# Kernel optimization log

Measured on AMD Instinct MI355X. Metric: run time of the kernel, lower is better.

The kernel has to match this reference:

```python
import jax, jax.numpy as jnp
import numpy as np

EPS = 1e-12  # matches torch.nn.functional.normalize default eps


def _l2norm_ch(x):
    # normalize over channel axis (dim=1), x: [B, D, N]
    n = jnp.sqrt(jnp.sum(x * x, axis=1, keepdims=True))
    return x / jnp.maximum(n, EPS)


def setup_inputs() -> dict:
    key = jax.random.key(0)
    k0, k1, kq, kk, kv = jax.random.split(key, 5)
    B, D, H, W = 8, 128, 64, 64
    return {
        "vol0": jax.random.normal(k0, (B, D, H, W), dtype=jnp.float32),
        "vol1": jax.random.normal(k1, (B, D, H, W), dtype=jnp.float32),
        "Wq": jax.random.normal(kq, (D, D), dtype=jnp.float32) * 0.05,
        "Wk": jax.random.normal(kk, (D, D), dtype=jnp.float32) * 0.05,
        "Wv": jax.random.normal(kv, (D, D), dtype=jnp.float32) * 0.05,
    }


def reference(vol0, vol1, Wq, Wk, Wv):
    B, D, H, W = vol0.shape
    N = H * W
    x0 = vol0.reshape(B, D, N)
    x1 = vol1.reshape(B, D, N)

    # 1x1 convs (bias=False) == channel matmuls; residual connections enabled
    q = jnp.einsum('od,bdn->bon', Wq, x0) + x0
    k = jnp.einsum('od,bdn->bon', Wk, x1) + x1
    v0 = jnp.einsum('od,bdn->bon', Wv, x0) + x0
    v1 = jnp.einsum('od,bdn->bon', Wv, x1) + x1

    # normalise dot product: L2-normalize over channel dim
    q = _l2norm_ch(q)
    k = _l2norm_ch(k)

    # correlation volume + row softmax: cvolume[b, n, m]
    cvolume = jax.nn.softmax(jnp.einsum('bdn,bdm->bnm', q, k), axis=2)

    # warp v1 by attention: v1w[b, d, n] = sum_m v1[b, d, m] * cvolume[b, n, m]
    v1w = jnp.einsum('bdm,bnm->bdn', v1, cvolume)

    # position encoder (meshgrid with 'ij' indexing, as legacy torch.meshgrid)
    u = jnp.linspace(-1.0, 1.0, H)
    v = jnp.linspace(-1.0, 1.0, W)
    uu, vv = jnp.meshgrid(u, v, indexing='ij')
    grid = jnp.stack([uu, vv], axis=0).reshape(2, N)  # [2, N]
    pos = jnp.einsum('cm,bnm->bcn', grid, cvolume)  # [B, 2, N]

    # max-score channel: [B, 1, N]
    max_score = jnp.max(cvolume, axis=2)[:, None, :]

    agg = jnp.concatenate([v0, v1w, pos, max_score], axis=1)  # [B, 2D+3, N]
    return agg.reshape(B, 2 * D + 3, H, W)
```

## Files before the change

kernel.cpp:

```cpp
#include <hip/hip_runtime.h>
#include <hip/hip_bf16.h>

#define B_   8
#define D_   128
#define N_   4096
#define CH   259

typedef short bf8 __attribute__((ext_vector_type(8)));
typedef float f4  __attribute__((ext_vector_type(4)));

typedef unsigned int as1_u32 __attribute__((address_space(1)));
typedef unsigned int as3_u32 __attribute__((address_space(3)));

__device__ __forceinline__ void gll16(const void* g, void* l) {
    __builtin_amdgcn_global_load_lds((as1_u32*)(unsigned long long)g,
                                     (as3_u32*)(unsigned int)(unsigned long long)l,
                                     16, 0, 0);
}

__device__ __forceinline__ unsigned short f2bf(float x) {
    unsigned int u = __float_as_uint(x);
    return (unsigned short)((u + 0x7FFFu + ((u >> 16) & 1u)) >> 16);
}

__device__ __forceinline__ unsigned int cvtpk(float lo, float hi) {
    unsigned int r;
    asm("v_cvt_pk_bf16_f32 %0, %1, %2" : "=v"(r) : "v"(lo), "v"(hi));
    return r;
}

__global__ void wconv_kernel(const float* __restrict__ Wq,
                             const float* __restrict__ Wk,
                             const float* __restrict__ Wv,
                             unsigned short* __restrict__ Wb) {
    const float* src = (blockIdx.x == 0) ? Wq : (blockIdx.x == 1) ? Wk : Wv;
    unsigned short* dst = Wb + (size_t)blockIdx.x * D_ * D_;
    for (int i = threadIdx.x; i < D_ * D_; i += blockDim.x) dst[i] = f2bf(src[i]);
}

__global__ __launch_bounds__(256, 2) void proj_kernel(
    const float* __restrict__ vol0, const float* __restrict__ vol1,
    const unsigned short* __restrict__ Wb, float* __restrict__ out,
    unsigned short* __restrict__ Qp, unsigned short* __restrict__ Kh,
    unsigned short* __restrict__ V2)
{
    __shared__ __align__(16) float xs[2][D_ * 64];

    const int tid  = threadIdx.x;
    const int wave = tid >> 6, lane = tid & 63;
    const int l15  = lane & 15, lh = lane >> 4;

    const int bid = blockIdx.x;
    const int swz = (bid & 7) * 64 + (bid >> 3);
    const int b   = swz >> 6;
    const int n0  = (swz & 63) * 64;

    #pragma unroll
    for (int a = 0; a < 2; ++a) {
        const char* src = (const char*)((a ? vol1 : vol0) + (size_t)b * D_ * N_ + n0);
        char* dstb = (char*)&xs[a][0];
        #pragma unroll
        for (int i = 0; i < 8; ++i) {
            int dst16 = i * 4096 + tid * 16;
            int row = dst16 >> 8, cb = dst16 & 255;
            gll16(src + (size_t)row * (N_ * 4) + (cb ^ (((row >> 3) & 7) << 4)), dstb + dst16);
        }
    }
    __syncthreads();

    const int nrow = wave * 16 + l15;

    auto afrag = [&](const float* base, int k) -> bf8 {
        const int dbase = k * 32 + lh * 8;
        const unsigned int cb = ((unsigned int)(nrow * 4)) ^ (((unsigned int)((k * 4 + lh) & 7)) << 4);
        const float* p = base + dbase * 64 + (cb >> 2);
        union { bf8 v; unsigned int w[4]; } u;
        #pragma unroll
        for (int jj = 0; jj < 4; ++jj)
            u.w[jj] = cvtpk(p[(2 * jj) * 64], p[(2 * jj + 1) * 64]);
        return u.v;
    };

    f4 aq[8], ak[8], a0v[8], a1v[8];
    #pragma unroll
    for (int ob = 0; ob < 8; ++ob) {
        aq[ob] = (f4){0.f,0.f,0.f,0.f}; ak[ob] = (f4){0.f,0.f,0.f,0.f};
        a0v[ob] = (f4){0.f,0.f,0.f,0.f}; a1v[ob] = (f4){0.f,0.f,0.f,0.f};
    }

    const unsigned short* Wqb = Wb;
    const unsigned short* Wkb = Wb + D_ * D_;
    const unsigned short* Wvb = Wb + 2 * D_ * D_;

    for (int k = 0; k < 4; ++k) {
        bf8 x0f = afrag(&xs[0][0], k);
        bf8 x1f = afrag(&xs[1][0], k);
        #pragma unroll
        for (int ob = 0; ob < 8; ++ob) {
            const size_t woff = ((size_t)(ob * 16 + l15)) * D_ + k * 32 + lh * 8;
            bf8 wq = *(const bf8*)(Wqb + woff);
            bf8 wk = *(const bf8*)(Wkb + woff);
            bf8 wv = *(const bf8*)(Wvb + woff);
            aq[ob]  = __builtin_amdgcn_mfma_f32_16x16x32_bf16(x0f, wq, aq[ob], 0, 0, 0);
            ak[ob]  = __builtin_amdgcn_mfma_f32_16x16x32_bf16(x1f, wk, ak[ob], 0, 0, 0);
            a0v[ob] = __builtin_amdgcn_mfma_f32_16x16x32_bf16(x0f, wv, a0v[ob], 0, 0, 0);
            a1v[ob] = __builtin_amdgcn_mfma_f32_16x16x32_bf16(x1f, wv, a1v[ob], 0, 0, 0);
        }
    }

    float ssq[4] = {0.f,0.f,0.f,0.f}, ssk[4] = {0.f,0.f,0.f,0.f};
    #pragma unroll
    for (int ob = 0; ob < 8; ++ob) {
        const int o = ob * 16 + l15;
        const unsigned int okey = (((unsigned int)((o >> 3) & 7)) << 4);
        #pragma unroll
        for (int r = 0; r < 4; ++r) {
            int n = wave * 16 + lh * 4 + r;
            int ci = o * 64 + (int)(((((unsigned int)(n * 4)) ^ okey) >> 2));
            float r0 = xs[0][ci], r1 = xs[1][ci];
            aq[ob][r] += r0; ak[ob][r] += r1; a0v[ob][r] += r0; a1v[ob][r] += r1;
            ssq[r] = fmaf(aq[ob][r], aq[ob][r], ssq[r]);
            ssk[r] = fmaf(ak[ob][r], ak[ob][r], ssk[r]);
        }
    }
    #pragma unroll
    for (int off = 1; off < 16; off <<= 1)
        #pragma unroll
        for (int r = 0; r < 4; ++r) {
            ssq[r] += __shfl_xor(ssq[r], off, 64);
            ssk[r] += __shfl_xor(ssk[r], off, 64);
        }
    float rq[4], rk[4];
    #pragma unroll
    for (int r = 0; r < 4; ++r) {
        rq[r] = 1.44269504088896f / fmaxf(sqrtf(ssq[r]), 1e-12f);
        rk[r] = 1.0f / fmaxf(sqrtf(ssk[r]), 1e-12f);
    }

    const int nbase = n0 + wave * 16 + lh * 4;
    char* v2chunk = (char*)V2 + ((size_t)(b * 128 + (nbase >> 5))) * 8192
                  + (nbase & 31) * 2;

    #pragma unroll
    for (int ob = 0; ob < 8; ++ob) {
        const int o = ob * 16 + l15;
        *(f4*)(out + ((size_t)(b * CH + o)) * N_ + nbase) = a0v[ob];
        uint2 pv; pv.x = cvtpk(a1v[ob][0], a1v[ob][1]); pv.y = cvtpk(a1v[ob][2], a1v[ob][3]);
        *(uint2*)(v2chunk + (size_t)o * 64) = pv;
        uint2 pq; pq.x = cvtpk(aq[ob][0]*rq[0], aq[ob][1]*rq[1]);
        pq.y = cvtpk(aq[ob][2]*rq[2], aq[ob][3]*rq[3]);
        *(uint2*)(Qp + ((size_t)(b * D_ + o)) * N_ + nbase) = pq;
    }

    __syncthreads();
    float* chunk = &xs[0][0] + wave * 2176;
    #pragma unroll
    for (int ob = 0; ob < 8; ++ob) {
        const int o = ob * 16 + l15;
        #pragma unroll
        for (int r = 0; r < 4; ++r) chunk[o * 17 + lh * 4 + r] = ak[ob][r] * rk[r];
    }
    asm volatile("s_waitcnt lgkmcnt(0)" ::: "memory");
    __builtin_amdgcn_sched_barrier(0);
    {
        const int o0 = (lane & 15) * 8, nr = lane >> 4;
        #pragma unroll
        for (int t = 0; t < 4; ++t) {
            int nl = t * 4 + nr;
            float f[8];
            #pragma unroll
            for (int j = 0; j < 8; ++j) f[j] = chunk[(o0 + j) * 17 + nl];
            uint4 st;
            st.x = cvtpk(f[0], f[1]); st.y = cvtpk(f[2], f[3]);
            st.z = cvtpk(f[4], f[5]); st.w = cvtpk(f[6], f[7]);
            *(uint4*)(Kh + ((size_t)(b * N_ + n0 + wave * 16 + nl)) * D_ + o0) = st;
        }
    }
}

__global__ __launch_bounds__(512, 2) void attn_kernel(
    const unsigned short* __restrict__ Qp, const unsigned short* __restrict__ Kh,
    const unsigned short* __restrict__ V2, float* __restrict__ out)
{
    __shared__ __align__(16) char smem[81920];
    char* KB = smem;
    char* VB = smem + 32768;
    char* PB = smem + 65536;

    const int tid  = threadIdx.x;
    const int wave = tid >> 6, lane = tid & 63;
    const int l15  = lane & 15, lh = lane >> 4;
    const int mhalf = wave & 1, qquad = wave >> 1;

    const int bid = blockIdx.x;
    const int swz = (bid & 7) * 32 + (bid >> 3);
    const int b   = swz >> 5;
    const int n0  = (swz & 31) * 128;
    const int nw  = n0 + qquad * 32;

    bf8 qf[2][4];
    const unsigned short* Qb = Qp + (size_t)b * D_ * N_;
    #pragma unroll
    for (int qg = 0; qg < 2; ++qg)
        #pragma unroll
        for (int dc = 0; dc < 4; ++dc) {
            union { bf8 v; unsigned short e[8]; } u;
            #pragma unroll
            for (int j = 0; j < 8; ++j)
                u.e[j] = Qb[((size_t)(dc * 32 + lh * 8 + j)) * N_ + nw + qg * 16 + l15];
            qf[qg][dc] = u.v;
        }

    f4 acc[2][8];
    #pragma unroll
    for (int qg = 0; qg < 2; ++qg)
        #pragma unroll
        for (int dc = 0; dc < 8; ++dc) acc[qg][dc] = (f4){0.f,0.f,0.f,0.f};
    float lsum[2] = {0.f, 0.f}, pu[2] = {0.f, 0.f}, pvv[2] = {0.f, 0.f};
    float Mp[2] = {-1e30f, -1e30f};

    float vb0[8];
    #pragma unroll
    for (int s = 0; s < 2; ++s)
        #pragma unroll
        for (int r = 0; r < 4; ++r)
            vb0[s * 4 + r] = -1.f + (2.f / 63.f) * (float)(s * 16 + lh * 4 + r);

    const char* Kbytes = (const char*)(Kh + (size_t)b * N_ * D_);
    const char* Vbytes = (const char*)V2 + ((size_t)b * 128) * 8192;
    char* Pw = PB + wave * 2048;

    const int sK = (wave < 4);
    const int smh = sK ? (wave >> 1) : ((wave - 4) >> 1);
    const int spt = sK ? (wave & 1) : ((wave - 4) & 1);
    unsigned int soffs[4];
    #pragma unroll
    for (int ii = 0; ii < 4; ++ii) {
        if (sK) {
            int rr = spt * 16 + ii * 4 + (lane >> 4);
            unsigned int col = (unsigned int)((lane & 15) * 16);
            soffs[ii] = (unsigned int)(rr * 256) + (col ^ (unsigned int)((rr & 7) << 4));
        } else {
            int vr = spt * 64 + ii * 16 + (lane >> 2);
            unsigned int mc = (unsigned int)((lane & 3) * 16);
            soffs[ii] = (unsigned int)(vr * 64) + (mc ^ (unsigned int)(((vr >> 1) & 3) << 4));
        }
    }
    auto stage = [&](int buf, int t) {
        if (sK) {
            const char* ks = Kbytes + (size_t)smh * 524288 + (size_t)t * 8192;
            char* kd = KB + buf * 16384 + smh * 8192 + spt * 4096;
            #pragma unroll
            for (int ii = 0; ii < 4; ++ii) gll16(ks + soffs[ii], kd + ii * 1024);
        } else {
            const char* vs = Vbytes + ((size_t)(smh * 64 + t)) * 8192;
            char* vd = VB + buf * 16384 + smh * 8192 + spt * 4096;
            #pragma unroll
            for (int ii = 0; ii < 4; ++ii) gll16(vs + soffs[ii], vd + ii * 1024);
        }
    };

    unsigned int kcol[4];
    #pragma unroll
    for (int dc = 0; dc < 4; ++dc)
        kcol[dc] = ((unsigned int)(dc * 64 + lh * 16)) ^ ((unsigned int)((l15 & 7) << 4));
    const unsigned int pkey  = ((unsigned int)((l15 >> 1) & 3)) << 4;
    const unsigned int prow0 = (unsigned int)(l15 * 64);
    const unsigned int prow1 = (unsigned int)((16 + l15) * 64);
    const unsigned int px    = ((unsigned int)(lh * 16)) ^ pkey;
    const unsigned int vxx   = ((unsigned int)(lh * 16)) ^ pkey;

    stage(0, 0);
    __syncthreads();

    for (int t = 0; t < 64; ++t) {
        const int cur = t & 1;
        if (t + 1 < 64) stage(cur ^ 1, t + 1);

        const char* Kc = KB + cur * 16384 + mhalf * 8192 + l15 * 256;
        const char* Vc = VB + cur * 16384 + mhalf * 8192 + l15 * 64 + vxx;
        const int c = mhalf * 64 + t;

        f4 s00 = (f4){0.f,0.f,0.f,0.f}, s01 = (f4){0.f,0.f,0.f,0.f};
        f4 s10 = (f4){0.f,0.f,0.f,0.f}, s11 = (f4){0.f,0.f,0.f,0.f};
        __builtin_amdgcn_s_setprio(1);
        #pragma unroll
        for (int dc = 0; dc < 4; ++dc) {
            bf8 k0 = *(const bf8*)(Kc + kcol[dc]);
            bf8 k1 = *(const bf8*)(Kc + 4096 + kcol[dc]);
            s00 = __builtin_amdgcn_mfma_f32_16x16x32_bf16(k0, qf[0][dc], s00, 0, 0, 0);
            s10 = __builtin_amdgcn_mfma_f32_16x16x32_bf16(k0, qf[1][dc], s10, 0, 0, 0);
            s01 = __builtin_amdgcn_mfma_f32_16x16x32_bf16(k1, qf[0][dc], s01, 0, 0, 0);
            s11 = __builtin_amdgcn_mfma_f32_16x16x32_bf16(k1, qf[1][dc], s11, 0, 0, 0);
        }
        __builtin_amdgcn_s_setprio(0);

        const float ut   = -1.f + (2.f / 63.f) * (float)(c >> 1);
        const float voff = (c & 1) ? (64.f / 63.f) : 0.f;
        #pragma unroll
        for (int qg = 0; qg < 2; ++qg) {
            f4 sa = qg ? s10 : s00, sb = qg ? s11 : s01;
            float p[8];
            #pragma unroll
            for (int r = 0; r < 4; ++r) {
                p[r]     = __builtin_amdgcn_exp2f(sa[r]);
                p[4 + r] = __builtin_amdgcn_exp2f(sb[r]);
            }
            Mp[qg] = fmaxf(Mp[qg], fmaxf(fmaxf(fmaxf(sa[0], sa[1]), fmaxf(sa[2], sa[3])),
                                         fmaxf(fmaxf(sb[0], sb[1]), fmaxf(sb[2], sb[3]))));
            float ps = ((p[0]+p[1]) + (p[2]+p[3])) + ((p[4]+p[5]) + (p[6]+p[7]));
            float pvp = 0.f;
            #pragma unroll
            for (int i = 0; i < 8; ++i) pvp = fmaf(vb0[i], p[i], pvp);
            lsum[qg] += ps;
            pu[qg]  = fmaf(ut, ps, pu[qg]);
            pvv[qg] = fmaf(voff, ps, pvv[qg] + pvp);
            const unsigned int pr = qg ? prow1 : prow0;
            uint2 w0; w0.x = cvtpk(p[0], p[1]); w0.y = cvtpk(p[2], p[3]);
            uint2 w1; w1.x = cvtpk(p[4], p[5]); w1.y = cvtpk(p[6], p[7]);
            *(uint2*)(Pw + pr + (((unsigned int)(lh * 8)) ^ pkey))      = w0;
            *(uint2*)(Pw + pr + (((unsigned int)(32 + lh * 8)) ^ pkey)) = w1;
        }
        asm volatile("s_waitcnt lgkmcnt(0)" ::: "memory");
        __builtin_amdgcn_sched_barrier(0);

        bf8 pf0 = *(const bf8*)(Pw + prow0 + px);
        bf8 pf1 = *(const bf8*)(Pw + prow1 + px);
        __builtin_amdgcn_s_setprio(1);
        #pragma unroll
        for (int dc = 0; dc < 8; ++dc) {
            bf8 vfd = *(const bf8*)(Vc + dc * 1024);
            acc[0][dc] = __builtin_amdgcn_mfma_f32_16x16x32_bf16(pf0, vfd, acc[0][dc], 0, 0, 0);
            acc[1][dc] = __builtin_amdgcn_mfma_f32_16x16x32_bf16(pf1, vfd, acc[1][dc], 0, 0, 0);
        }
        __builtin_amdgcn_s_setprio(0);
        __syncthreads();
    }

    #pragma unroll
    for (int qg = 0; qg < 2; ++qg) {
        #pragma unroll
        for (int off = 16; off < 64; off <<= 1) {
            lsum[qg] += __shfl_xor(lsum[qg], off, 64);
            pu[qg]   += __shfl_xor(pu[qg], off, 64);
            pvv[qg]  += __shfl_xor(pvv[qg], off, 64);
            Mp[qg]    = fmaxf(Mp[qg], __shfl_xor(Mp[qg], off, 64));
        }
    }

    __syncthreads();
    float* ex  = (float*)smem;
    float* stt = (float*)(smem + 69632);
    if (lane < 16) {
        #pragma unroll
        for (int qg = 0; qg < 2; ++qg) {
            float* s = stt + ((wave * 2 + qg) * 16 + l15) * 4;
            s[0] = lsum[qg]; s[1] = pu[qg]; s[2] = pvv[qg]; s[3] = Mp[qg];
        }
    }
    #pragma unroll
    for (int qg = 0; qg < 2; ++qg)
        #pragma unroll
        for (int j = 0; j < 4; ++j) {
            float* e = ex + (((wave * 2 + qg) * 4 + j) * 16 + lh * 4) * 17 + l15;
            if (mhalf == 0) {
                #pragma unroll
                for (int r = 0; r < 4; ++r) e[r * 17] = acc[qg][4 + j][r];
            } else {
                #pragma unroll
                for (int r = 0; r < 4; ++r) e[r * 17] = acc[qg][j][r];
            }
        }
    __syncthreads();

    const int pw_ = wave ^ 1;
    float rl[2], PUm[2], PVm[2], Mm[2];
    #pragma unroll
    for (int qg = 0; qg < 2; ++qg) {
        const float* s = stt + ((pw_ * 2 + qg) * 16 + l15) * 4;
        float Lm = lsum[qg] + s[0];
        PUm[qg] = pu[qg]  + s[1];
        PVm[qg] = pvv[qg] + s[2];
        Mm[qg]  = fmaxf(Mp[qg], s[3]);
        rl[qg]  = __builtin_amdgcn_rcpf(Lm);
    }

    #pragma unroll
    for (int qg = 0; qg < 2; ++qg) {
        float rlr[4];
        #pragma unroll
        for (int r = 0; r < 4; ++r)
            rlr[r] = __shfl(rl[qg], (lane & 48) + lh * 4 + r, 64);
        #pragma unroll
        for (int j = 0; j < 4; ++j) {
            const float* e = ex + (((pw_ * 2 + qg) * 4 + j) * 16 + lh * 4) * 17 + l15;
            f4 v;
            if (mhalf == 0) {
                #pragma unroll
                for (int r = 0; r < 4; ++r) v[r] = (acc[qg][j][r] + e[r * 17]) * rlr[r];
            } else {
                #pragma unroll
                for (int r = 0; r < 4; ++r) v[r] = (acc[qg][4 + j][r] + e[r * 17]) * rlr[r];
            }
            const int och = 128 + (mhalf * 4 + j) * 16 + l15;
            *(f4*)(out + ((size_t)(b * CH + och)) * N_ + nw + qg * 16 + lh * 4) = v;
        }
    }
    if (mhalf == 0 && lh == 0) {
        #pragma unroll
        for (int qg = 0; qg < 2; ++qg) {
            const int gn = nw + qg * 16 + l15;
            out[((size_t)(b * CH + 256)) * N_ + gn] = PUm[qg] * rl[qg];
            out[((size_t)(b * CH + 257)) * N_ + gn] = PVm[qg] * rl[qg];
            out[((size_t)(b * CH + 258)) * N_ + gn] =
                __builtin_amdgcn_exp2f(Mm[qg]) * rl[qg];
        }
    }
}

extern "C" void kernel_launch(void* const* d_in, const int* in_sizes, int n_in,
                              void* d_out, int out_size, void* d_ws, size_t ws_size,
                              hipStream_t stream) {
    const float* vol0 = (const float*)d_in[0];
    const float* vol1 = (const float*)d_in[1];
    const float* Wq   = (const float*)d_in[2];
    const float* Wk   = (const float*)d_in[3];
    const float* Wv   = (const float*)d_in[4];
    float* out = (float*)d_out;

    char* ws = (char*)d_ws;
    const size_t QP_BYTES  = (size_t)B_ * D_ * N_ * 2;
    const size_t KH_BYTES  = (size_t)B_ * N_ * D_ * 2;
    const size_t V2_BYTES  = (size_t)B_ * D_ * N_ * 2;
    unsigned short* Qp  = (unsigned short*)(ws);
    unsigned short* Kh  = (unsigned short*)(ws + QP_BYTES);
    unsigned short* V2  = (unsigned short*)(ws + QP_BYTES + KH_BYTES);
    unsigned short* Wb  = (unsigned short*)(ws + QP_BYTES + KH_BYTES + V2_BYTES);

    hipLaunchKernelGGL(wconv_kernel, dim3(3), dim3(256), 0, stream, Wq, Wk, Wv, Wb);
    hipLaunchKernelGGL(proj_kernel, dim3(512), dim3(256), 0, stream,
                       vol0, vol1, Wb, out, Qp, Kh, V2);
    hipLaunchKernelGGL(attn_kernel, dim3(256), dim3(512), 0, stream,
                       Qp, Kh, V2, out);
}
```

Measured before the change: 141.0 us.

## Software-pipeline PV MFMA one step behind QK MFMA in attention loop

Restructures the main loop so each iteration's P and V fragments are loaded into registers at the end of the previous step. The P·V MFMAs for tile t-1 are then issued right after the QK MFMAs for tile t, followed by a peeled epilogue for the last tile. The aim is to keep the matrix cores busy while the exp/softmax VALU work and the LDS stores run, and to hide LDS read latency. In exchange it holds more live registers (eight V fragments plus preloaded K fragments), which may lower occupancy or cause spills, and it moves the global-to-LDS staging later in the iteration.

```diff
diff --git a/kernel.cpp b/kernel.cpp
--- a/kernel.cpp
+++ b/kernel.cpp
@@ -268,33 +268,8 @@
     const unsigned int prow0 = (unsigned int)(l15 * 64);
     const unsigned int prow1 = (unsigned int)((16 + l15) * 64);
     const unsigned int px    = ((unsigned int)(lh * 16)) ^ pkey;
-    const unsigned int vxx   = ((unsigned int)(lh * 16)) ^ pkey;
-
-    stage(0, 0);
-    __syncthreads();
-
-    for (int t = 0; t < 64; ++t) {
-        const int cur = t & 1;
-        if (t + 1 < 64) stage(cur ^ 1, t + 1);
-
-        const char* Kc = KB + cur * 16384 + mhalf * 8192 + l15 * 256;
-        const char* Vc = VB + cur * 16384 + mhalf * 8192 + l15 * 64 + vxx;
-        const int c = mhalf * 64 + t;
-
-        f4 s00 = (f4){0.f,0.f,0.f,0.f}, s01 = (f4){0.f,0.f,0.f,0.f};
-        f4 s10 = (f4){0.f,0.f,0.f,0.f}, s11 = (f4){0.f,0.f,0.f,0.f};
-        __builtin_amdgcn_s_setprio(1);
-        #pragma unroll
-        for (int dc = 0; dc < 4; ++dc) {
-            bf8 k0 = *(const bf8*)(Kc + kcol[dc]);
-            bf8 k1 = *(const bf8*)(Kc + 4096 + kcol[dc]);
-            s00 = __builtin_amdgcn_mfma_f32_16x16x32_bf16(k0, qf[0][dc], s00, 0, 0, 0);
-            s10 = __builtin_amdgcn_mfma_f32_16x16x32_bf16(k0, qf[1][dc], s10, 0, 0, 0);
-            s01 = __builtin_amdgcn_mfma_f32_16x16x32_bf16(k1, qf[0][dc], s01, 0, 0, 0);
-            s11 = __builtin_amdgcn_mfma_f32_16x16x32_bf16(k1, qf[1][dc], s11, 0, 0, 0);
-        }
-        __builtin_amdgcn_s_setprio(0);
-
+
+    auto softmax_store = [&](int c, f4 s00, f4 s01, f4 s10, f4 s11) {
         const float ut   = -1.f + (2.f / 63.f) * (float)(c >> 1);
         const float voff = (c & 1) ? (64.f / 63.f) : 0.f;
         #pragma unroll
@@ -321,21 +296,90 @@
             *(uint2*)(Pw + pr + (((unsigned int)(lh * 8)) ^ pkey))      = w0;
             *(uint2*)(Pw + pr + (((unsigned int)(32 + lh * 8)) ^ pkey)) = w1;
         }
+    };
+
+    bf8 pfA, pfB, vfc[8];
+
+    stage(0, 0);
+    __syncthreads();
+
+    {
+        const char* Kc = KB + mhalf * 8192 + l15 * 256;
+        const char* Vc = VB + mhalf * 8192 + l15 * 64 + px;
+        f4 s00 = (f4){0.f,0.f,0.f,0.f}, s01 = (f4){0.f,0.f,0.f,0.f};
+        f4 s10 = (f4){0.f,0.f,0.f,0.f}, s11 = (f4){0.f,0.f,0.f,0.f};
+        __builtin_amdgcn_s_setprio(1);
+        #pragma unroll
+        for (int dc = 0; dc < 4; ++dc) {
+            bf8 k0 = *(const bf8*)(Kc + kcol[dc]);
+            bf8 k1 = *(const bf8*)(Kc + 4096 + kcol[dc]);
+            s00 = __builtin_amdgcn_mfma_f32_16x16x32_bf16(k0, qf[0][dc], s00, 0, 0, 0);
+            s10 = __builtin_amdgcn_mfma_f32_16x16x32_bf16(k0, qf[1][dc], s10, 0, 0, 0);
+            s01 = __builtin_amdgcn_mfma_f32_16x16x32_bf16(k1, qf[0][dc], s01, 0, 0, 0);
+            s11 = __builtin_amdgcn_mfma_f32_16x16x32_bf16(k1, qf[1][dc], s11, 0, 0, 0);
+        }
+        __builtin_amdgcn_s_setprio(0);
+        softmax_store(mhalf * 64, s00, s01, s10, s11);
+        stage(1, 1);
         asm volatile("s_waitcnt lgkmcnt(0)" ::: "memory");
         __builtin_amdgcn_sched_barrier(0);
-
-        bf8 pf0 = *(const bf8*)(Pw + prow0 + px);
-        bf8 pf1 = *(const bf8*)(Pw + prow1 + px);
+        pfA = *(const bf8*)(Pw + prow0 + px);
+        pfB = *(const bf8*)(Pw + prow1 + px);
+        #pragma unroll
+        for (int dc = 0; dc < 8; ++dc) vfc[dc] = *(const bf8*)(Vc + dc * 1024);
+        __syncthreads();
+    }
+
+    for (int t = 1; t < 64; ++t) {
+        const int cur = t & 1;
+        const char* Kc = KB + cur * 16384 + mhalf * 8192 + l15 * 256;
+        const char* Vc = VB + cur * 16384 + mhalf * 8192 + l15 * 64 + px;
+        const int c = mhalf * 64 + t;
+
+        bf8 k0[4], k1[4];
+        #pragma unroll
+        for (int dc = 0; dc < 4; ++dc) {
+            k0[dc] = *(const bf8*)(Kc + kcol[dc]);
+            k1[dc] = *(const bf8*)(Kc + 4096 + kcol[dc]);
+        }
+
+        f4 s00 = (f4){0.f,0.f,0.f,0.f}, s01 = (f4){0.f,0.f,0.f,0.f};
+        f4 s10 = (f4){0.f,0.f,0.f,0.f}, s11 = (f4){0.f,0.f,0.f,0.f};
         __builtin_amdgcn_s_setprio(1);
         #pragma unroll
+        for (int dc = 0; dc < 4; ++dc) {
+            s00 = __builtin_amdgcn_mfma_f32_16x16x32_bf16(k0[dc], qf[0][dc], s00, 0, 0, 0);
+            s10 = __builtin_amdgcn_mfma_f32_16x16x32_bf16(k0[dc], qf[1][dc], s10, 0, 0, 0);
+            s01 = __builtin_amdgcn_mfma_f32_16x16x32_bf16(k1[dc], qf[0][dc], s01, 0, 0, 0);
+            s11 = __builtin_amdgcn_mfma_f32_16x16x32_bf16(k1[dc], qf[1][dc], s11, 0, 0, 0);
+        }
+        #pragma unroll
         for (int dc = 0; dc < 8; ++dc) {
-            bf8 vfd = *(const bf8*)(Vc + dc * 1024);
-            acc[0][dc] = __builtin_amdgcn_mfma_f32_16x16x32_bf16(pf0, vfd, acc[0][dc], 0, 0, 0);
-            acc[1][dc] = __builtin_amdgcn_mfma_f32_16x16x32_bf16(pf1, vfd, acc[1][dc], 0, 0, 0);
+            acc[0][dc] = __builtin_amdgcn_mfma_f32_16x16x32_bf16(pfA, vfc[dc], acc[0][dc], 0, 0, 0);
+            acc[1][dc] = __builtin_amdgcn_mfma_f32_16x16x32_bf16(pfB, vfc[dc], acc[1][dc], 0, 0, 0);
         }
         __builtin_amdgcn_s_setprio(0);
+
+        softmax_store(c, s00, s01, s10, s11);
+
+        if (t < 63) stage(cur ^ 1, t + 1);
+
+        asm volatile("s_waitcnt lgkmcnt(0)" ::: "memory");
+        __builtin_amdgcn_sched_barrier(0);
+        pfA = *(const bf8*)(Pw + prow0 + px);
+        pfB = *(const bf8*)(Pw + prow1 + px);
+        #pragma unroll
+        for (int dc = 0; dc < 8; ++dc) vfc[dc] = *(const bf8*)(Vc + dc * 1024);
         __syncthreads();
     }
+
+    __builtin_amdgcn_s_setprio(1);
+    #pragma unroll
+    for (int dc = 0; dc < 8; ++dc) {
+        acc[0][dc] = __builtin_amdgcn_mfma_f32_16x16x32_bf16(pfA, vfc[dc], acc[0][dc], 0, 0, 0);
+        acc[1][dc] = __builtin_amdgcn_mfma_f32_16x16x32_bf16(pfB, vfc[dc], acc[1][dc], 0, 0, 0);
+    }
+    __builtin_amdgcn_s_setprio(0);
 
     #pragma unroll
     for (int qg = 0; qg < 2; ++qg) {
```

Result: slower. 144.7 us (+2.6%).

## Pipeline projection input staging with MFMA and parallelize weight conversion

Applied to the files above, without the earlier changes.

The proj kernel now stages its input tile in four slices, loading later slices while computing MFMAs on the earlier ones, and uses a new LDS swizzle key. The residual add reads directly from global memory instead of LDS. The weight conversion kernel is spread over 48 blocks with vectorized float4 loads and packed bf16 conversion. The aim is to hide load latency and shorten the tiny serial prologue kernel, at the cost of extra barriers and duplicate global reads.

```diff
diff --git a/kernel.cpp b/kernel.cpp
--- a/kernel.cpp
+++ b/kernel.cpp
@@ -18,24 +18,22 @@
                                      16, 0, 0);
 }
 
-__device__ __forceinline__ unsigned short f2bf(float x) {
-    unsigned int u = __float_as_uint(x);
-    return (unsigned short)((u + 0x7FFFu + ((u >> 16) & 1u)) >> 16);
-}
-
 __device__ __forceinline__ unsigned int cvtpk(float lo, float hi) {
     unsigned int r;
     asm("v_cvt_pk_bf16_f32 %0, %1, %2" : "=v"(r) : "v"(lo), "v"(hi));
     return r;
 }
 
-__global__ void wconv_kernel(const float* __restrict__ Wq,
-                             const float* __restrict__ Wk,
-                             const float* __restrict__ Wv,
-                             unsigned short* __restrict__ Wb) {
-    const float* src = (blockIdx.x == 0) ? Wq : (blockIdx.x == 1) ? Wk : Wv;
-    unsigned short* dst = Wb + (size_t)blockIdx.x * D_ * D_;
-    for (int i = threadIdx.x; i < D_ * D_; i += blockDim.x) dst[i] = f2bf(src[i]);
+__global__ __launch_bounds__(256) void wconv_kernel(
+    const float* __restrict__ Wq, const float* __restrict__ Wk,
+    const float* __restrict__ Wv, unsigned short* __restrict__ Wb) {
+    const int idx = blockIdx.x * 256 + threadIdx.x;
+    const int which = idx >> 12;
+    const int e4 = idx & 4095;
+    const float* src = (which == 0) ? Wq : (which == 1) ? Wk : Wv;
+    float4 v = *(const float4*)(src + e4 * 4);
+    uint2 o; o.x = cvtpk(v.x, v.y); o.y = cvtpk(v.z, v.w);
+    *(uint2*)(Wb + ((size_t)which << 14) + e4 * 4) = o;
 }
 
 __global__ __launch_bounds__(256, 2) void proj_kernel(
@@ -55,24 +53,29 @@
     const int b   = swz >> 6;
     const int n0  = (swz & 63) * 64;
 
-    #pragma unroll
-    for (int a = 0; a < 2; ++a) {
-        const char* src = (const char*)((a ? vol1 : vol0) + (size_t)b * D_ * N_ + n0);
-        char* dstb = (char*)&xs[a][0];
-        #pragma unroll
-        for (int i = 0; i < 8; ++i) {
-            int dst16 = i * 4096 + tid * 16;
-            int row = dst16 >> 8, cb = dst16 & 255;
-            gll16(src + (size_t)row * (N_ * 4) + (cb ^ (((row >> 3) & 7) << 4)), dstb + dst16);
-        }
-    }
-    __syncthreads();
+    auto stageslice = [&](int s) {
+        #pragma unroll
+        for (int a = 0; a < 2; ++a) {
+            const char* src = (const char*)((a ? vol1 : vol0) + (size_t)b * D_ * N_ + n0);
+            char* dstb = (char*)&xs[a][0];
+            #pragma unroll
+            for (int i = 0; i < 2; ++i) {
+                int dst16 = (2 * s + i) * 4096 + tid * 16;
+                int row = dst16 >> 8, cb = dst16 & 255;
+                int rg = row >> 3;
+                unsigned int key = (unsigned int)(((rg & 3) | ((rg & 1) << 2)) << 4);
+                gll16(src + (size_t)row * (N_ * 4) + (cb ^ key), dstb + dst16);
+            }
+        }
+    };
 
     const int nrow = wave * 16 + l15;
 
     auto afrag = [&](const float* base, int k) -> bf8 {
         const int dbase = k * 32 + lh * 8;
-        const unsigned int cb = ((unsigned int)(nrow * 4)) ^ (((unsigned int)((k * 4 + lh) & 7)) << 4);
+        const int rg = dbase >> 3;
+        const unsigned int key = (unsigned int)(((rg & 3) | ((rg & 1) << 2)) << 4);
+        const unsigned int cb = ((unsigned int)(nrow * 4)) ^ key;
         const float* p = base + dbase * 64 + (cb >> 2);
         union { bf8 v; unsigned int w[4]; } u;
         #pragma unroll
@@ -92,7 +95,13 @@
     const unsigned short* Wkb = Wb + D_ * D_;
     const unsigned short* Wvb = Wb + 2 * D_ * D_;
 
+    stageslice(0);
+    stageslice(1);
+    __syncthreads();
+
+    #pragma unroll
     for (int k = 0; k < 4; ++k) {
+        if (k < 2) stageslice(k + 2);
         bf8 x0f = afrag(&xs[0][0], k);
         bf8 x1f = afrag(&xs[1][0], k);
         #pragma unroll
@@ -106,19 +115,20 @@
             a0v[ob] = __builtin_amdgcn_mfma_f32_16x16x32_bf16(x0f, wv, a0v[ob], 0, 0, 0);
             a1v[ob] = __builtin_amdgcn_mfma_f32_16x16x32_bf16(x1f, wv, a1v[ob], 0, 0, 0);
         }
-    }
-
+        if (k < 2) __syncthreads();
+    }
+
+    const int nbase = n0 + wave * 16 + lh * 4;
     float ssq[4] = {0.f,0.f,0.f,0.f}, ssk[4] = {0.f,0.f,0.f,0.f};
     #pragma unroll
     for (int ob = 0; ob < 8; ++ob) {
         const int o = ob * 16 + l15;
-        const unsigned int okey = (((unsigned int)((o >> 3) & 7)) << 4);
+        f4 r0 = *(const f4*)(vol0 + ((size_t)(b * D_ + o)) * N_ + nbase);
+        f4 r1 = *(const f4*)(vol1 + ((size_t)(b * D_ + o)) * N_ + nbase);
         #pragma unroll
         for (int r = 0; r < 4; ++r) {
-            int n = wave * 16 + lh * 4 + r;
-            int ci = o * 64 + (int)(((((unsigned int)(n * 4)) ^ okey) >> 2));
-            float r0 = xs[0][ci], r1 = xs[1][ci];
-            aq[ob][r] += r0; ak[ob][r] += r1; a0v[ob][r] += r0; a1v[ob][r] += r1;
+            aq[ob][r] += r0[r]; ak[ob][r] += r1[r];
+            a0v[ob][r] += r0[r]; a1v[ob][r] += r1[r];
             ssq[r] = fmaf(aq[ob][r], aq[ob][r], ssq[r]);
             ssk[r] = fmaf(ak[ob][r], ak[ob][r], ssk[r]);
         }
@@ -137,7 +147,6 @@
         rk[r] = 1.0f / fmaxf(sqrtf(ssk[r]), 1e-12f);
     }
 
-    const int nbase = n0 + wave * 16 + lh * 4;
     char* v2chunk = (char*)V2 + ((size_t)(b * 128 + (nbase >> 5))) * 8192
                   + (nbase & 31) * 2;
 
@@ -437,7 +446,7 @@
     unsigned short* V2  = (unsigned short*)(ws + QP_BYTES + KH_BYTES);
     unsigned short* Wb  = (unsigned short*)(ws + QP_BYTES + KH_BYTES + V2_BYTES);
 
-    hipLaunchKernelGGL(wconv_kernel, dim3(3), dim3(256), 0, stream, Wq, Wk, Wv, Wb);
+    hipLaunchKernelGGL(wconv_kernel, dim3(48), dim3(256), 0, stream, Wq, Wk, Wv, Wb);
     hipLaunchKernelGGL(proj_kernel, dim3(512), dim3(256), 0, stream,
                        vol0, vol1, Wb, out, Qp, Kh, V2);
     hipLaunchKernelGGL(attn_kernel, dim3(256), dim3(512), 0, stream,
```

Measured after the change: 124.5 us, median of 2. 11.7% less time.
